# Kernel tuning notes

Measured on AMD Instinct MI355X. Metric: run time of the kernel, lower is better.

Reference implementation:

```python
import jax, jax.numpy as jnp
import numpy as np

B, IN, H = 4096, 1024, 4096
EPS = 1e-5

def setup_inputs() -> dict:
    key = jax.random.key(0)
    ks = jax.random.split(key, 20)
    std = 0.01
    inp = {
        "input": jax.random.normal(ks[0], (B, IN), jnp.float32),
        "max_v": jnp.ones((1,), jnp.float32),
        "min_v": jnp.zeros((1,), jnp.float32),
        "hidden": jax.random.normal(ks[1], (B, 1, H), jnp.float32),
        "Wr_w": std * jax.random.normal(ks[2], (H, IN), jnp.float32),
        "Wr_b": std * jax.random.normal(ks[3], (H,), jnp.float32),
        "Ur_w": std * jax.random.normal(ks[4], (H, H), jnp.float32),
        "Ur_b": std * jax.random.normal(ks[5], (H,), jnp.float32),
        "Wz_w": std * jax.random.normal(ks[6], (H, IN), jnp.float32),
        "Wz_b": std * jax.random.normal(ks[7], (H,), jnp.float32),
        "Uz_w": std * jax.random.normal(ks[8], (H, H), jnp.float32),
        "Uz_b": std * jax.random.normal(ks[9], (H,), jnp.float32),
        "Wh_w": std * jax.random.normal(ks[10], (H, IN), jnp.float32),
        "Wh_b": std * jax.random.normal(ks[11], (H,), jnp.float32),
        "Uh_w": std * jax.random.normal(ks[12], (H, H), jnp.float32),
        "Uh_b": std * jax.random.normal(ks[13], (H,), jnp.float32),
        "out_w": std * jax.random.normal(ks[14], (4, H), jnp.float32),
        "out_b": std * jax.random.normal(ks[15], (4,), jnp.float32),
        "bn_gamma": jnp.ones((1,), jnp.float32),
        "bn_beta": jnp.zeros((1,), jnp.float32),
    }
    return inp

def _lin(x, W, b):
    # x: [B,1,F], W: [O,F] -> [B,1,O]
    return jnp.einsum('blf,of->blo', x, W) + b

def reference(input, max_v, min_v, hidden, Wr_w, Wr_b, Ur_w, Ur_b, Wz_w, Wz_b,
              Uz_w, Uz_b, Wh_w, Wh_b, Uh_w, Uh_b, out_w, out_b, bn_gamma, bn_beta):
    x = input[:, None, :]  # [B,1,IN]
    reset_gate = jax.nn.sigmoid(_lin(x, Wr_w, Wr_b) + _lin(hidden, Ur_w, Ur_b))
    update_gate = jax.nn.sigmoid(_lin(x, Wz_w, Wz_b) + _lin(hidden, Uz_w, Uz_b))
    h_pre = _lin(x, Wh_w, Wh_b) + reset_gate * _lin(hidden, Uh_w, Uh_b)  # [B,1,H]
    # BatchNorm1d(1) in training mode: single channel -> normalize over ALL elements
    mean = jnp.mean(h_pre)
    var = jnp.mean(jnp.square(h_pre - mean))  # biased variance (torch norm uses biased)
    h_bn = (h_pre - mean) * jax.lax.rsqrt(var + EPS) * bn_gamma[0] + bn_beta[0]
    proposal = jax.nn.relu(h_bn)
    current_state = (1.0 - update_gate) * hidden + update_gate * proposal  # [B,1,H]
    out = jnp.einsum('blh,oh->blo', current_state, out_w) + out_b  # [B,1,4]
    return (current_state, out[:, :, 0], out[:, :, 1], out[:, :, 2], out[:, :, 3])
```

## Files before the change

kernel.cpp:

```cpp
#include <hip/hip_runtime.h>

#define HH 4096
#define BB 4096
#define IND 1024
#define NTOT 16777216
#define EPSV 1e-5f

typedef unsigned short u16;
typedef __bf16 bf16x8 __attribute__((ext_vector_type(8)));
typedef float f32x4 __attribute__((ext_vector_type(4)));
typedef u16 u16x8 __attribute__((ext_vector_type(8)));

__device__ __forceinline__ u16 f2bf(float f) {
    unsigned u = __builtin_bit_cast(unsigned, f);
    u += 0x7fffu + ((u >> 16) & 1u);
    return (u16)(u >> 16);
}
__device__ __forceinline__ float bf2f(u16 h) {
    return __builtin_bit_cast(float, ((unsigned)h) << 16);
}

__global__ void cvt_kernel(const float* __restrict__ src, u16* __restrict__ dst, int n) {
    int i4 = (blockIdx.x * blockDim.x + threadIdx.x) * 4;
    int stride = gridDim.x * blockDim.x * 4;
    for (; i4 < n; i4 += stride) {
        f32x4 v = *(const f32x4*)(src + i4);
        u16 o0 = f2bf(v[0]), o1 = f2bf(v[1]), o2 = f2bf(v[2]), o3 = f2bf(v[3]);
        unsigned p0 = (unsigned)o0 | ((unsigned)o1 << 16);
        unsigned p1 = (unsigned)o2 | ((unsigned)o3 << 16);
        *(uint2*)(dst + i4) = make_uint2(p0, p1);
    }
}


__device__ __forceinline__ void stage_tile(const u16* __restrict__ g, int ld, int row0, int k0,
                                           u16* lds, int tid) {
    int l = tid & 63, w = tid >> 6;
#pragma unroll
    for (int jr = 0; jr < 4; ++jr) {
        int offw = jr * 4096 + w * 1024;
        int offl = offw + l * 16;
        int row = offl >> 7;
        int kb = offl & 127;
        const u16* ga = g + (size_t)(row0 + row) * ld + (k0 + (kb >> 1));
        __builtin_amdgcn_global_load_lds(
            (const __attribute__((address_space(1))) unsigned*)ga,
            (__attribute__((address_space(3))) unsigned*)(lds + (offw >> 1)),
            16, 0, 0);
    }
}

__device__ __forceinline__ void zero_acc(f32x4 (&acc)[4][4]) {
#pragma unroll
    for (int i = 0; i < 4; ++i)
#pragma unroll
        for (int j = 0; j < 4; ++j) {
            f32x4 zz = {0.f, 0.f, 0.f, 0.f};
            acc[i][j] = zz;
        }
}

__device__ __forceinline__ void run_phase(const u16* __restrict__ A, int row0a,
                                          const u16* __restrict__ B, int ld, int Klen,
                                          u16* Alds, u16* Blds,
                                          f32x4 (&acc)[4][4], int tid) {
    const int l = tid & 63;
    const int wid = tid >> 6;
    const int wr = wid >> 1, wc = wid & 1;
    const int arow = wr * 64 + (l & 15);
    const int brow = wc * 64 + (l & 15);
    const int kcol = (l >> 4) * 8;
    for (int k0 = 0; k0 < Klen; k0 += 64) {
        stage_tile(A, ld, row0a, k0, Alds, tid);
        stage_tile(B, ld, 0, k0, Blds, tid);
        __syncthreads();
#pragma unroll
        for (int kk = 0; kk < 2; ++kk) {
            bf16x8 af[4], bfr[4];
#pragma unroll
            for (int i = 0; i < 4; ++i)
                af[i] = *(const bf16x8*)(Alds + (arow + i * 16) * 64 + kk * 32 + kcol);
#pragma unroll
            for (int j = 0; j < 4; ++j)
                bfr[j] = *(const bf16x8*)(Blds + (brow + j * 16) * 64 + kk * 32 + kcol);
#pragma unroll
            for (int i = 0; i < 4; ++i)
#pragma unroll
                for (int j = 0; j < 4; ++j)
                    acc[i][j] = __builtin_amdgcn_mfma_f32_16x16x32_bf16(af[i], bfr[j], acc[i][j], 0, 0, 0);
        }
        __syncthreads();
    }
}

__global__ __launch_bounds__(256, 2) void gru_gemm(
    const u16* __restrict__ xbf, const u16* __restrict__ hbf,
    const u16* __restrict__ Wr, const u16* __restrict__ Ur,
    const u16* __restrict__ Wz, const u16* __restrict__ Uz,
    const u16* __restrict__ Wh, const u16* __restrict__ Uh,
    const float* __restrict__ Wr_b, const float* __restrict__ Ur_b,
    const float* __restrict__ Wz_b, const float* __restrict__ Uz_b,
    const float* __restrict__ Wh_b, const float* __restrict__ Uh_b,
    u16* __restrict__ z_out, u16* __restrict__ hpre_out, float* __restrict__ partials) {
    __shared__ __align__(16) u16 Alds[128 * 64];
    __shared__ __align__(16) u16 Blds[128 * 64];
    __shared__ float redS[4], redSS[4];

    const int tid = threadIdx.x;
    const int m0 = blockIdx.x * 128, n0 = blockIdx.y * 128;
    const int l = tid & 63, wid = tid >> 6;
    const int wr = wid >> 1, wc = wid & 1;

    f32x4 acc[4][4];

    zero_acc(acc);
    run_phase(xbf, m0, Wr + (size_t)n0 * IND, IND, IND, Alds, Blds, acc, tid);
    run_phase(hbf, m0, Ur + (size_t)n0 * HH, HH, HH, Alds, Blds, acc, tid);

    float r_st[4][4][4];
#pragma unroll
    for (int j = 0; j < 4; ++j) {
        int col = n0 + wc * 64 + j * 16 + (l & 15);
        float bias = __ldg(Wr_b + col) + __ldg(Ur_b + col);
#pragma unroll
        for (int i = 0; i < 4; ++i)
#pragma unroll
            for (int q = 0; q < 4; ++q)
                r_st[i][j][q] = 1.f / (1.f + __expf(-(acc[i][j][q] + bias)));
    }

    zero_acc(acc);
    run_phase(xbf, m0, Wz + (size_t)n0 * IND, IND, IND, Alds, Blds, acc, tid);
    run_phase(hbf, m0, Uz + (size_t)n0 * HH, HH, HH, Alds, Blds, acc, tid);
#pragma unroll
    for (int j = 0; j < 4; ++j) {
        int col = n0 + wc * 64 + j * 16 + (l & 15);
        float bias = __ldg(Wz_b + col) + __ldg(Uz_b + col);
#pragma unroll
        for (int i = 0; i < 4; ++i) {
            int rowb = m0 + wr * 64 + i * 16 + (l >> 4) * 4;
#pragma unroll
            for (int q = 0; q < 4; ++q) {
                float zv = 1.f / (1.f + __expf(-(acc[i][j][q] + bias)));
                z_out[(size_t)(rowb + q) * HH + col] = f2bf(zv);
            }
        }
    }

    zero_acc(acc);
    run_phase(hbf, m0, Uh + (size_t)n0 * HH, HH, HH, Alds, Blds, acc, tid);
#pragma unroll
    for (int j = 0; j < 4; ++j) {
        int col = n0 + wc * 64 + j * 16 + (l & 15);
        float bias = __ldg(Uh_b + col);
#pragma unroll
        for (int i = 0; i < 4; ++i)
#pragma unroll
            for (int q = 0; q < 4; ++q)
                acc[i][j][q] = r_st[i][j][q] * (acc[i][j][q] + bias);
    }
    run_phase(xbf, m0, Wh + (size_t)n0 * IND, IND, IND, Alds, Blds, acc, tid);

    float s = 0.f, ss = 0.f;
#pragma unroll
    for (int j = 0; j < 4; ++j) {
        int col = n0 + wc * 64 + j * 16 + (l & 15);
        float bias = __ldg(Wh_b + col);
#pragma unroll
        for (int i = 0; i < 4; ++i) {
            int rowb = m0 + wr * 64 + i * 16 + (l >> 4) * 4;
#pragma unroll
            for (int q = 0; q < 4; ++q) {
                float hv = acc[i][j][q] + bias;
                hpre_out[(size_t)(rowb + q) * HH + col] = f2bf(hv);
                s += hv;
                ss += hv * hv;
            }
        }
    }
#pragma unroll
    for (int off = 32; off; off >>= 1) {
        s += __shfl_down(s, off, 64);
        ss += __shfl_down(ss, off, 64);
    }
    if (l == 0) { redS[wid] = s; redSS[wid] = ss; }
    __syncthreads();
    if (tid == 0) {
        int bid = blockIdx.y * gridDim.x + blockIdx.x;
        partials[2 * bid] = redS[0] + redS[1] + redS[2] + redS[3];
        partials[2 * bid + 1] = redSS[0] + redSS[1] + redSS[2] + redSS[3];
    }
}

__global__ void reduce_stats(const float* __restrict__ partials, int nblk,
                             const float* __restrict__ gamma, const float* __restrict__ beta,
                             float* __restrict__ stats) {
    __shared__ float rs[4], rss[4];
    int tid = threadIdx.x;
    float s = 0.f, ss = 0.f;
    for (int i = tid; i < nblk; i += blockDim.x) {
        s += partials[2 * i];
        ss += partials[2 * i + 1];
    }
#pragma unroll
    for (int off = 32; off; off >>= 1) {
        s += __shfl_down(s, off, 64);
        ss += __shfl_down(ss, off, 64);
    }
    if ((tid & 63) == 0) { rs[tid >> 6] = s; rss[tid >> 6] = ss; }
    __syncthreads();
    if (tid == 0) {
        float S = rs[0] + rs[1] + rs[2] + rs[3];
        float SS = rss[0] + rss[1] + rss[2] + rss[3];
        float mean = S / (float)NTOT;
        float var = SS / (float)NTOT - mean * mean;
        float scale = gamma[0] * rsqrtf(var + EPSV);
        stats[0] = scale;
        stats[1] = beta[0] - mean * scale;
    }
}

__global__ __launch_bounds__(256) void finalize(
    const u16* __restrict__ z, const u16* __restrict__ hpre,
    const float* __restrict__ hidden, const float* __restrict__ out_w,
    const float* __restrict__ out_b, const float* __restrict__ stats,
    float* __restrict__ d_out) {
    __shared__ float red[4][4];
    const int b = blockIdx.x, t = threadIdx.x;
    const float scale = stats[0], shift = stats[1];
    const size_t row = (size_t)b * HH;
    float so[4] = {0.f, 0.f, 0.f, 0.f};
#pragma unroll
    for (int jj = 0; jj < 2; ++jj) {
        int h0 = jj * 2048 + t * 8;
        u16x8 zv = *(const u16x8*)(z + row + h0);
        u16x8 hp = *(const u16x8*)(hpre + row + h0);
        f32x4 hd0 = *(const f32x4*)(hidden + row + h0);
        f32x4 hd1 = *(const f32x4*)(hidden + row + h0 + 4);
        f32x4 o0, o1;
#pragma unroll
        for (int e = 0; e < 8; ++e) {
            float zf = bf2f(zv[e]);
            float pv = bf2f(hp[e]) * scale + shift;
            pv = pv > 0.f ? pv : 0.f;
            float hf = (e < 4) ? hd0[e] : hd1[e - 4];
            float cs = (1.f - zf) * hf + zf * pv;
            if (e < 4) o0[e] = cs; else o1[e - 4] = cs;
#pragma unroll
            for (int o = 0; o < 4; ++o)
                so[o] += cs * __ldg(out_w + o * HH + h0 + e);
        }
        *(f32x4*)(d_out + row + h0) = o0;
        *(f32x4*)(d_out + row + h0 + 4) = o1;
    }
#pragma unroll
    for (int off = 32; off; off >>= 1)
#pragma unroll
        for (int o = 0; o < 4; ++o) so[o] += __shfl_down(so[o], off, 64);
    if ((t & 63) == 0)
#pragma unroll
        for (int o = 0; o < 4; ++o) red[t >> 6][o] = so[o];
    __syncthreads();
    if (t < 4) {
        float v = red[0][t] + red[1][t] + red[2][t] + red[3][t] + __ldg(out_b + t);
        d_out[(size_t)NTOT + (size_t)t * BB + b] = v;
    }
}

extern "C" void kernel_launch(void* const* d_in, const int* in_sizes, int n_in,
                              void* d_out, int out_size, void* d_ws, size_t ws_size,
                              hipStream_t stream) {
    const float* input = (const float*)d_in[0];
    const float* hidden = (const float*)d_in[3];
    const float* Wr_w = (const float*)d_in[4];  const float* Wr_b = (const float*)d_in[5];
    const float* Ur_w = (const float*)d_in[6];  const float* Ur_b = (const float*)d_in[7];
    const float* Wz_w = (const float*)d_in[8];  const float* Wz_b = (const float*)d_in[9];
    const float* Uz_w = (const float*)d_in[10]; const float* Uz_b = (const float*)d_in[11];
    const float* Wh_w = (const float*)d_in[12]; const float* Wh_b = (const float*)d_in[13];
    const float* Uh_w = (const float*)d_in[14]; const float* Uh_b = (const float*)d_in[15];
    const float* out_w = (const float*)d_in[16]; const float* out_b = (const float*)d_in[17];
    const float* gamma = (const float*)d_in[18]; const float* beta = (const float*)d_in[19];

    char* ws = (char*)d_ws;
    size_t off = 0;
    auto alloc = [&](size_t bytes) {
        void* p = ws + off;
        off = (off + bytes + 255) & ~(size_t)255;
        return p;
    };
    u16* xbf = (u16*)alloc((size_t)BB * IND * 2);
    u16* hbf = (u16*)alloc((size_t)BB * HH * 2);
    u16* wr = (u16*)alloc((size_t)HH * IND * 2);
    u16* wz = (u16*)alloc((size_t)HH * IND * 2);
    u16* wh = (u16*)alloc((size_t)HH * IND * 2);
    u16* ur = (u16*)alloc((size_t)HH * HH * 2);
    u16* uz = (u16*)alloc((size_t)HH * HH * 2);
    u16* uh = (u16*)alloc((size_t)HH * HH * 2);
    u16* zpl = (u16*)alloc((size_t)BB * HH * 2);
    u16* hpl = (u16*)alloc((size_t)BB * HH * 2);
    float* partials = (float*)alloc(2048 * sizeof(float));
    float* stats = (float*)alloc(16);

    cvt_kernel<<<512, 256, 0, stream>>>(input, xbf, BB * IND);
    cvt_kernel<<<2048, 256, 0, stream>>>(hidden, hbf, BB * HH);
    cvt_kernel<<<512, 256, 0, stream>>>(Wr_w, wr, HH * IND);
    cvt_kernel<<<512, 256, 0, stream>>>(Wz_w, wz, HH * IND);
    cvt_kernel<<<512, 256, 0, stream>>>(Wh_w, wh, HH * IND);
    cvt_kernel<<<2048, 256, 0, stream>>>(Ur_w, ur, HH * HH);
    cvt_kernel<<<2048, 256, 0, stream>>>(Uz_w, uz, HH * HH);
    cvt_kernel<<<2048, 256, 0, stream>>>(Uh_w, uh, HH * HH);

    gru_gemm<<<dim3(32, 32), 256, 0, stream>>>(xbf, hbf, wr, ur, wz, uz, wh, uh,
                                               Wr_b, Ur_b, Wz_b, Uz_b, Wh_b, Uh_b,
                                               zpl, hpl, partials);
    reduce_stats<<<1, 256, 0, stream>>>(partials, 1024, gamma, beta, stats);
    finalize<<<BB, 256, 0, stream>>>(zpl, hpl, hidden, out_w, out_b, stats, (float*)d_out);
}
```

Before: 867.1 us.

## Split fused GRU GEMM into three 256x256-tile pipelined GEMM kernels

Replaces the single fused 128x128-tile kernel, which computed all three gates in sequence, with three launches of a templated 256x256-tile, 512-thread GEMM. The new GEMM uses 128KB of dynamic LDS with double buffering, a swizzled layout, and interleaved global-to-LDS staging with priority-boosted MFMA phases. The reset gate is written as a bf16 plane into the output buffer and read back in the h_pre epilogue. Larger tiles raise arithmetic intensity and the prefetch pipeline hides load latency. The cost is extra global traffic for the r plane and lower occupancy per CU.

```diff
diff --git a/kernel.cpp b/kernel.cpp
--- a/kernel.cpp
+++ b/kernel.cpp
@@ -33,162 +33,229 @@
 }
 
 
-__device__ __forceinline__ void stage_tile(const u16* __restrict__ g, int ld, int row0, int k0,
-                                           u16* lds, int tid) {
-    int l = tid & 63, w = tid >> 6;
-#pragma unroll
-    for (int jr = 0; jr < 4; ++jr) {
-        int offw = jr * 4096 + w * 1024;
-        int offl = offw + l * 16;
-        int row = offl >> 7;
-        int kb = offl & 127;
-        const u16* ga = g + (size_t)(row0 + row) * ld + (k0 + (kb >> 1));
-        __builtin_amdgcn_global_load_lds(
-            (const __attribute__((address_space(1))) unsigned*)ga,
-            (__attribute__((address_space(3))) unsigned*)(lds + (offw >> 1)),
-            16, 0, 0);
-    }
-}
-
-__device__ __forceinline__ void zero_acc(f32x4 (&acc)[4][4]) {
-#pragma unroll
-    for (int i = 0; i < 4; ++i)
+__device__ __forceinline__ int lds_off(int r, int c) {
+    int sub = ((r >> 4) << 1) | (c >> 5);
+    int lin = ((r & 15) << 6) | ((c & 31) << 1);
+    lin ^= (r & 8) << 2;
+    return ((sub << 10) | lin) >> 1;
+}
+
+template<int NT1, int NT2, int EPI>
+__global__ __launch_bounds__(512, 2) void gemm256(
+    const u16* __restrict__ A0, const u16* __restrict__ B0,
+    const u16* __restrict__ A1, const u16* __restrict__ B1,
+    const float* __restrict__ bias_a, const float* __restrict__ bias_b,
+    const u16* __restrict__ rplane, u16* __restrict__ outp,
+    float* __restrict__ partials) {
+    constexpr int NT = NT1 + NT2;
+    constexpr int LD0 = (EPI == 2) ? HH : IND;
+    constexpr int LD1 = (EPI == 2) ? IND : HH;
+    extern __shared__ __align__(16) u16 smem[];
+
+    const int tid = threadIdx.x;
+    const int l = tid & 63, w = tid >> 6;
+    const int lr = l & 15, lq = l >> 4;
+    const int wr = w >> 2;
+    const int wn = w & 3;
+    const int bh = wn >> 1;
+    const int m0 = blockIdx.x * 256, n0 = blockIdx.y * 256;
+    const int linh = ((((lr << 6) | (lq << 4)) ^ ((lr & 8) << 2)) >> 1);
+    const int bsub0 = (wn & 1) * 4;
+
+    auto stageTile = [&](int tt, int mat, int h) {
+        const u16* g = (tt < NT1) ? (mat ? B0 : A0) : (mat ? B1 : A1);
+        const int ld = (tt < NT1) ? LD0 : LD1;
+        const int kb = ((tt < NT1) ? tt : tt - NT1) * 64;
+        const int rowbase = (mat ? n0 : m0) + h * 128;
+        u16* base = smem + (tt & 1) * 32768 + mat * 16384 + h * 8192;
+        const int wq = l << 4;
+        const int lin = wq ^ (((wq >> 9) & 1) << 5);
+        const int rl = lin >> 6;
+        const int cl = (lin & 63) >> 1;
+#pragma unroll
+        for (int j = 0; j < 2; ++j) {
+            const int sub = j * 8 + w;
+            const int r = ((sub >> 1) << 4) | rl;
+            const int c0 = ((sub & 1) << 5) | cl;
+            const u16* ga = g + (size_t)(rowbase + r) * ld + (kb + c0);
+            __builtin_amdgcn_global_load_lds(
+                (const __attribute__((address_space(1))) unsigned*)ga,
+                (__attribute__((address_space(3))) unsigned*)(base + (sub << 9)),
+                16, 0, 0);
+        }
+    };
+
+    f32x4 acc[8][4];
+#pragma unroll
+    for (int i = 0; i < 8; ++i)
 #pragma unroll
         for (int j = 0; j < 4; ++j) {
             f32x4 zz = {0.f, 0.f, 0.f, 0.f};
             acc[i][j] = zz;
         }
-}
-
-__device__ __forceinline__ void run_phase(const u16* __restrict__ A, int row0a,
-                                          const u16* __restrict__ B, int ld, int Klen,
-                                          u16* Alds, u16* Blds,
-                                          f32x4 (&acc)[4][4], int tid) {
-    const int l = tid & 63;
-    const int wid = tid >> 6;
-    const int wr = wid >> 1, wc = wid & 1;
-    const int arow = wr * 64 + (l & 15);
-    const int brow = wc * 64 + (l & 15);
-    const int kcol = (l >> 4) * 8;
-    for (int k0 = 0; k0 < Klen; k0 += 64) {
-        stage_tile(A, ld, row0a, k0, Alds, tid);
-        stage_tile(B, ld, 0, k0, Blds, tid);
+
+    stageTile(0, 0, 0); stageTile(0, 0, 1); stageTile(0, 1, 0); stageTile(0, 1, 1);
+    stageTile(1, 0, 0); stageTile(1, 0, 1);
+    asm volatile("s_waitcnt vmcnt(4)" ::: "memory");
+    __builtin_amdgcn_s_barrier();
+
+    bf16x8 a0[4][2], a1[4][2], bb[2][2];
+
+    for (int t = 0; t < NT; ++t) {
+        const u16* Ah = smem + (t & 1) * 32768 + wr * 8192 + linh;
+        const u16* Bh = smem + (t & 1) * 32768 + 16384 + bh * 8192 + linh;
+        int t1 = t + 1; if (t1 == NT) t1 = 0;
+        int t2 = t + 2; if (t2 >= NT) t2 -= NT;
+
+#pragma unroll
+        for (int i = 0; i < 4; ++i)
+#pragma unroll
+            for (int ks = 0; ks < 2; ++ks)
+                a0[i][ks] = *(const bf16x8*)(Ah + (i * 2 + ks) * 512);
+#pragma unroll
+        for (int n = 0; n < 2; ++n)
+#pragma unroll
+            for (int ks = 0; ks < 2; ++ks)
+                bb[n][ks] = *(const bf16x8*)(Bh + ((bsub0 + n) * 2 + ks) * 512);
+        stageTile(t1, 1, 0);
+        __builtin_amdgcn_s_barrier();
+        asm volatile("s_waitcnt lgkmcnt(0)" ::: "memory");
+        __builtin_amdgcn_sched_barrier(0);
+        __builtin_amdgcn_s_setprio(1);
+#pragma unroll
+        for (int ks = 0; ks < 2; ++ks)
+#pragma unroll
+            for (int i = 0; i < 4; ++i)
+#pragma unroll
+                for (int n = 0; n < 2; ++n)
+                    acc[i][n] = __builtin_amdgcn_mfma_f32_16x16x32_bf16(a0[i][ks], bb[n][ks], acc[i][n], 0, 0, 0);
+        __builtin_amdgcn_s_setprio(0);
+        __builtin_amdgcn_s_barrier();
+
+#pragma unroll
+        for (int i = 0; i < 4; ++i)
+#pragma unroll
+            for (int ks = 0; ks < 2; ++ks)
+                a1[i][ks] = *(const bf16x8*)(Ah + 4096 + (i * 2 + ks) * 512);
+        stageTile(t1, 1, 1);
+        __builtin_amdgcn_s_barrier();
+        asm volatile("s_waitcnt lgkmcnt(0)" ::: "memory");
+        __builtin_amdgcn_sched_barrier(0);
+        __builtin_amdgcn_s_setprio(1);
+#pragma unroll
+        for (int ks = 0; ks < 2; ++ks)
+#pragma unroll
+            for (int i = 0; i < 4; ++i)
+#pragma unroll
+                for (int n = 0; n < 2; ++n)
+                    acc[4 + i][n] = __builtin_amdgcn_mfma_f32_16x16x32_bf16(a1[i][ks], bb[n][ks], acc[4 + i][n], 0, 0, 0);
+        __builtin_amdgcn_s_setprio(0);
+        __builtin_amdgcn_s_barrier();
+
+#pragma unroll
+        for (int n = 0; n < 2; ++n)
+#pragma unroll
+            for (int ks = 0; ks < 2; ++ks)
+                bb[n][ks] = *(const bf16x8*)(Bh + ((bsub0 + 2 + n) * 2 + ks) * 512);
+        stageTile(t2, 0, 0);
+        __builtin_amdgcn_s_barrier();
+        asm volatile("s_waitcnt lgkmcnt(0)" ::: "memory");
+        __builtin_amdgcn_sched_barrier(0);
+        __builtin_amdgcn_s_setprio(1);
+#pragma unroll
+        for (int ks = 0; ks < 2; ++ks)
+#pragma unroll
+            for (int i = 0; i < 4; ++i)
+#pragma unroll
+                for (int n = 0; n < 2; ++n)
+                    acc[i][2 + n] = __builtin_amdgcn_mfma_f32_16x16x32_bf16(a0[i][ks], bb[n][ks], acc[i][2 + n], 0, 0, 0);
+        __builtin_amdgcn_s_setprio(0);
+        __builtin_amdgcn_s_barrier();
+
+        stageTile(t2, 0, 1);
+        asm volatile("s_waitcnt vmcnt(4)" ::: "memory");
+        __builtin_amdgcn_s_barrier();
+        __builtin_amdgcn_s_setprio(1);
+#pragma unroll
+        for (int ks = 0; ks < 2; ++ks)
+#pragma unroll
+            for (int i = 0; i < 4; ++i)
+#pragma unroll
+                for (int n = 0; n < 2; ++n)
+                    acc[4 + i][2 + n] = __builtin_amdgcn_mfma_f32_16x16x32_bf16(a1[i][ks], bb[n][ks], acc[4 + i][2 + n], 0, 0, 0);
+        __builtin_amdgcn_s_setprio(0);
+        if constexpr (EPI == 2) {
+            if (t == NT1 - 1) {
+#pragma unroll
+                for (int m8 = 0; m8 < 8; ++m8) {
+                    const int rowb = m0 + wr * 128 + m8 * 16 + lq * 4;
+#pragma unroll
+                    for (int n8 = 0; n8 < 4; ++n8) {
+                        const int col = n0 + wn * 64 + n8 * 16 + lr;
+                        const float bias = bias_a[col];
+#pragma unroll
+                        for (int q = 0; q < 4; ++q) {
+                            float rv = bf2f(rplane[(size_t)(rowb + q) * HH + col]);
+                            acc[m8][n8][q] = rv * (acc[m8][n8][q] + bias);
+                        }
+                    }
+                }
+            }
+        }
+        __builtin_amdgcn_s_barrier();
+    }
+
+    if constexpr (EPI == 2) {
+        float s = 0.f, ss = 0.f;
+#pragma unroll
+        for (int m8 = 0; m8 < 8; ++m8) {
+            const int rowb = m0 + wr * 128 + m8 * 16 + lq * 4;
+#pragma unroll
+            for (int n8 = 0; n8 < 4; ++n8) {
+                const int col = n0 + wn * 64 + n8 * 16 + lr;
+                const float bias = bias_b[col];
+#pragma unroll
+                for (int q = 0; q < 4; ++q) {
+                    float v = acc[m8][n8][q] + bias;
+                    outp[(size_t)(rowb + q) * HH + col] = f2bf(v);
+                    s += v; ss += v * v;
+                }
+            }
+        }
+#pragma unroll
+        for (int off = 32; off; off >>= 1) {
+            s += __shfl_down(s, off, 64);
+            ss += __shfl_down(ss, off, 64);
+        }
+        asm volatile("s_waitcnt vmcnt(0)" ::: "memory");
         __syncthreads();
-#pragma unroll
-        for (int kk = 0; kk < 2; ++kk) {
-            bf16x8 af[4], bfr[4];
-#pragma unroll
-            for (int i = 0; i < 4; ++i)
-                af[i] = *(const bf16x8*)(Alds + (arow + i * 16) * 64 + kk * 32 + kcol);
-#pragma unroll
-            for (int j = 0; j < 4; ++j)
-                bfr[j] = *(const bf16x8*)(Blds + (brow + j * 16) * 64 + kk * 32 + kcol);
-#pragma unroll
-            for (int i = 0; i < 4; ++i)
-#pragma unroll
-                for (int j = 0; j < 4; ++j)
-                    acc[i][j] = __builtin_amdgcn_mfma_f32_16x16x32_bf16(af[i], bfr[j], acc[i][j], 0, 0, 0);
-        }
+        float* red = (float*)smem;
+        if (l == 0) { red[w * 2] = s; red[w * 2 + 1] = ss; }
         __syncthreads();
-    }
-}
-
-__global__ __launch_bounds__(256, 2) void gru_gemm(
-    const u16* __restrict__ xbf, const u16* __restrict__ hbf,
-    const u16* __restrict__ Wr, const u16* __restrict__ Ur,
-    const u16* __restrict__ Wz, const u16* __restrict__ Uz,
-    const u16* __restrict__ Wh, const u16* __restrict__ Uh,
-    const float* __restrict__ Wr_b, const float* __restrict__ Ur_b,
-    const float* __restrict__ Wz_b, const float* __restrict__ Uz_b,
-    const float* __restrict__ Wh_b, const float* __restrict__ Uh_b,
-    u16* __restrict__ z_out, u16* __restrict__ hpre_out, float* __restrict__ partials) {
-    __shared__ __align__(16) u16 Alds[128 * 64];
-    __shared__ __align__(16) u16 Blds[128 * 64];
-    __shared__ float redS[4], redSS[4];
-
-    const int tid = threadIdx.x;
-    const int m0 = blockIdx.x * 128, n0 = blockIdx.y * 128;
-    const int l = tid & 63, wid = tid >> 6;
-    const int wr = wid >> 1, wc = wid & 1;
-
-    f32x4 acc[4][4];
-
-    zero_acc(acc);
-    run_phase(xbf, m0, Wr + (size_t)n0 * IND, IND, IND, Alds, Blds, acc, tid);
-    run_phase(hbf, m0, Ur + (size_t)n0 * HH, HH, HH, Alds, Blds, acc, tid);
-
-    float r_st[4][4][4];
-#pragma unroll
-    for (int j = 0; j < 4; ++j) {
-        int col = n0 + wc * 64 + j * 16 + (l & 15);
-        float bias = __ldg(Wr_b + col) + __ldg(Ur_b + col);
-#pragma unroll
-        for (int i = 0; i < 4; ++i)
-#pragma unroll
-            for (int q = 0; q < 4; ++q)
-                r_st[i][j][q] = 1.f / (1.f + __expf(-(acc[i][j][q] + bias)));
-    }
-
-    zero_acc(acc);
-    run_phase(xbf, m0, Wz + (size_t)n0 * IND, IND, IND, Alds, Blds, acc, tid);
-    run_phase(hbf, m0, Uz + (size_t)n0 * HH, HH, HH, Alds, Blds, acc, tid);
-#pragma unroll
-    for (int j = 0; j < 4; ++j) {
-        int col = n0 + wc * 64 + j * 16 + (l & 15);
-        float bias = __ldg(Wz_b + col) + __ldg(Uz_b + col);
-#pragma unroll
-        for (int i = 0; i < 4; ++i) {
-            int rowb = m0 + wr * 64 + i * 16 + (l >> 4) * 4;
-#pragma unroll
-            for (int q = 0; q < 4; ++q) {
-                float zv = 1.f / (1.f + __expf(-(acc[i][j][q] + bias)));
-                z_out[(size_t)(rowb + q) * HH + col] = f2bf(zv);
+        if (tid == 0) {
+            float S = 0.f, SS = 0.f;
+#pragma unroll
+            for (int i = 0; i < 8; ++i) { S += red[2 * i]; SS += red[2 * i + 1]; }
+            const int bid = blockIdx.y * 16 + blockIdx.x;
+            partials[2 * bid] = S;
+            partials[2 * bid + 1] = SS;
+        }
+    } else {
+#pragma unroll
+        for (int m8 = 0; m8 < 8; ++m8) {
+            const int rowb = m0 + wr * 128 + m8 * 16 + lq * 4;
+#pragma unroll
+            for (int n8 = 0; n8 < 4; ++n8) {
+                const int col = n0 + wn * 64 + n8 * 16 + lr;
+                const float bias = bias_a[col] + bias_b[col];
+#pragma unroll
+                for (int q = 0; q < 4; ++q) {
+                    float v = 1.f / (1.f + __expf(-(acc[m8][n8][q] + bias)));
+                    outp[(size_t)(rowb + q) * HH + col] = f2bf(v);
+                }
             }
         }
-    }
-
-    zero_acc(acc);
-    run_phase(hbf, m0, Uh + (size_t)n0 * HH, HH, HH, Alds, Blds, acc, tid);
-#pragma unroll
-    for (int j = 0; j < 4; ++j) {
-        int col = n0 + wc * 64 + j * 16 + (l & 15);
-        float bias = __ldg(Uh_b + col);
-#pragma unroll
-        for (int i = 0; i < 4; ++i)
-#pragma unroll
-            for (int q = 0; q < 4; ++q)
-                acc[i][j][q] = r_st[i][j][q] * (acc[i][j][q] + bias);
-    }
-    run_phase(xbf, m0, Wh + (size_t)n0 * IND, IND, IND, Alds, Blds, acc, tid);
-
-    float s = 0.f, ss = 0.f;
-#pragma unroll
-    for (int j = 0; j < 4; ++j) {
-        int col = n0 + wc * 64 + j * 16 + (l & 15);
-        float bias = __ldg(Wh_b + col);
-#pragma unroll
-        for (int i = 0; i < 4; ++i) {
-            int rowb = m0 + wr * 64 + i * 16 + (l >> 4) * 4;
-#pragma unroll
-            for (int q = 0; q < 4; ++q) {
-                float hv = acc[i][j][q] + bias;
-                hpre_out[(size_t)(rowb + q) * HH + col] = f2bf(hv);
-                s += hv;
-                ss += hv * hv;
-            }
-        }
-    }
-#pragma unroll
-    for (int off = 32; off; off >>= 1) {
-        s += __shfl_down(s, off, 64);
-        ss += __shfl_down(ss, off, 64);
-    }
-    if (l == 0) { redS[wid] = s; redSS[wid] = ss; }
-    __syncthreads();
-    if (tid == 0) {
-        int bid = blockIdx.y * gridDim.x + blockIdx.x;
-        partials[2 * bid] = redS[0] + redS[1] + redS[2] + redS[3];
-        partials[2 * bid + 1] = redSS[0] + redSS[1] + redSS[2] + redSS[3];
+        asm volatile("s_waitcnt vmcnt(0)" ::: "memory");
     }
 }
 
@@ -290,29 +357,39 @@
     };
     u16* xbf = (u16*)alloc((size_t)BB * IND * 2);
     u16* hbf = (u16*)alloc((size_t)BB * HH * 2);
-    u16* wr = (u16*)alloc((size_t)HH * IND * 2);
-    u16* wz = (u16*)alloc((size_t)HH * IND * 2);
-    u16* wh = (u16*)alloc((size_t)HH * IND * 2);
-    u16* ur = (u16*)alloc((size_t)HH * HH * 2);
-    u16* uz = (u16*)alloc((size_t)HH * HH * 2);
-    u16* uh = (u16*)alloc((size_t)HH * HH * 2);
+    u16* wrp = (u16*)alloc((size_t)HH * IND * 2);
+    u16* wzp = (u16*)alloc((size_t)HH * IND * 2);
+    u16* whp = (u16*)alloc((size_t)HH * IND * 2);
+    u16* urp = (u16*)alloc((size_t)HH * HH * 2);
+    u16* uzp = (u16*)alloc((size_t)HH * HH * 2);
+    u16* uhp = (u16*)alloc((size_t)HH * HH * 2);
     u16* zpl = (u16*)alloc((size_t)BB * HH * 2);
     u16* hpl = (u16*)alloc((size_t)BB * HH * 2);
     float* partials = (float*)alloc(2048 * sizeof(float));
     float* stats = (float*)alloc(16);
 
+    u16* rpl = (u16*)d_out;
+
+    hipFuncSetAttribute((const void*)gemm256<16, 64, 0>, hipFuncAttributeMaxDynamicSharedMemorySize, 131072);
+    hipFuncSetAttribute((const void*)gemm256<16, 64, 1>, hipFuncAttributeMaxDynamicSharedMemorySize, 131072);
+    hipFuncSetAttribute((const void*)gemm256<64, 16, 2>, hipFuncAttributeMaxDynamicSharedMemorySize, 131072);
+
     cvt_kernel<<<512, 256, 0, stream>>>(input, xbf, BB * IND);
     cvt_kernel<<<2048, 256, 0, stream>>>(hidden, hbf, BB * HH);
-    cvt_kernel<<<512, 256, 0, stream>>>(Wr_w, wr, HH * IND);
-    cvt_kernel<<<512, 256, 0, stream>>>(Wz_w, wz, HH * IND);
-    cvt_kernel<<<512, 256, 0, stream>>>(Wh_w, wh, HH * IND);
-    cvt_kernel<<<2048, 256, 0, stream>>>(Ur_w, ur, HH * HH);
-    cvt_kernel<<<2048, 256, 0, stream>>>(Uz_w, uz, HH * HH);
-    cvt_kernel<<<2048, 256, 0, stream>>>(Uh_w, uh, HH * HH);
-
-    gru_gemm<<<dim3(32, 32), 256, 0, stream>>>(xbf, hbf, wr, ur, wz, uz, wh, uh,
-                                               Wr_b, Ur_b, Wz_b, Uz_b, Wh_b, Uh_b,
-                                               zpl, hpl, partials);
-    reduce_stats<<<1, 256, 0, stream>>>(partials, 1024, gamma, beta, stats);
+    cvt_kernel<<<512, 256, 0, stream>>>(Wr_w, wrp, HH * IND);
+    cvt_kernel<<<512, 256, 0, stream>>>(Wz_w, wzp, HH * IND);
+    cvt_kernel<<<512, 256, 0, stream>>>(Wh_w, whp, HH * IND);
+    cvt_kernel<<<2048, 256, 0, stream>>>(Ur_w, urp, HH * HH);
+    cvt_kernel<<<2048, 256, 0, stream>>>(Uz_w, uzp, HH * HH);
+    cvt_kernel<<<2048, 256, 0, stream>>>(Uh_w, uhp, HH * HH);
+
+    gemm256<16, 64, 0><<<dim3(16, 16), 512, 131072, stream>>>(
+        xbf, wrp, hbf, urp, Wr_b, Ur_b, nullptr, rpl, partials);
+    gemm256<16, 64, 1><<<dim3(16, 16), 512, 131072, stream>>>(
+        xbf, wzp, hbf, uzp, Wz_b, Uz_b, nullptr, zpl, partials);
+    gemm256<64, 16, 2><<<dim3(16, 16), 512, 131072, stream>>>(
+        hbf, uhp, xbf, whp, Uh_b, Wh_b, rpl, hpl, partials);
+
+    reduce_stats<<<1, 256, 0, stream>>>(partials, 256, gamma, beta, stats);
     finalize<<<BB, 256, 0, stream>>>(zpl, hpl, hidden, out_w, out_b, stats, (float*)d_out);
 }
```

New measurement: 827.9 us. 4.5% less time.

## Swizzle LDS tile layout and remap workgroups across XCDs in GRU GEMM

Applied to the files above, without the earlier changes.

Stores each staged tile in LDS as 16x32 sub-blocks with an XOR swizzle and rewrites the fragment reads to match. The goal is to remove bank conflicts on the bf16x8 reads that feed the MFMA instructions. The launch becomes a 1D grid, and each block index is remapped so that consecutive blocks dispatched to the same XCD share output tiles, which should improve L2 reuse of the A and B operands. The address math is subtle, so a swizzle mismatch would silently give wrong results.

```diff
diff --git a/kernel.cpp b/kernel.cpp
--- a/kernel.cpp
+++ b/kernel.cpp
@@ -35,17 +35,18 @@
 
 __device__ __forceinline__ void stage_tile(const u16* __restrict__ g, int ld, int row0, int k0,
                                            u16* lds, int tid) {
-    int l = tid & 63, w = tid >> 6;
-#pragma unroll
-    for (int jr = 0; jr < 4; ++jr) {
-        int offw = jr * 4096 + w * 1024;
-        int offl = offw + l * 16;
-        int row = offl >> 7;
-        int kb = offl & 127;
-        const u16* ga = g + (size_t)(row0 + row) * ld + (k0 + (kb >> 1));
+    const int l = tid & 63, w = tid >> 6;
+#pragma unroll
+    for (int j = 0; j < 4; ++j) {
+        const int sub = j * 4 + w;
+        const int d = l << 4;
+        const int lin = d ^ (((d >> 9) & 1) << 5);
+        const int r = ((sub >> 1) << 4) | (lin >> 6);
+        const int c = ((sub & 1) << 5) | ((lin & 63) >> 1);
+        const u16* ga = g + (size_t)(row0 + r) * ld + (k0 + c);
         __builtin_amdgcn_global_load_lds(
             (const __attribute__((address_space(1))) unsigned*)ga,
-            (__attribute__((address_space(3))) unsigned*)(lds + (offw >> 1)),
+            (__attribute__((address_space(3))) unsigned*)(lds + (sub << 9)),
             16, 0, 0);
     }
 }
@@ -67,9 +68,8 @@
     const int l = tid & 63;
     const int wid = tid >> 6;
     const int wr = wid >> 1, wc = wid & 1;
-    const int arow = wr * 64 + (l & 15);
-    const int brow = wc * 64 + (l & 15);
-    const int kcol = (l >> 4) * 8;
+    const int lr = l & 15, lq = l >> 4;
+    const int swzh = (((lr << 6) | (lq << 4)) ^ ((lr & 8) << 2)) >> 1;
     for (int k0 = 0; k0 < Klen; k0 += 64) {
         stage_tile(A, ld, row0a, k0, Alds, tid);
         stage_tile(B, ld, 0, k0, Blds, tid);
@@ -79,10 +79,10 @@
             bf16x8 af[4], bfr[4];
 #pragma unroll
             for (int i = 0; i < 4; ++i)
-                af[i] = *(const bf16x8*)(Alds + (arow + i * 16) * 64 + kk * 32 + kcol);
+                af[i] = *(const bf16x8*)(Alds + ((wr * 8 + i * 2 + kk) << 9) + swzh);
 #pragma unroll
             for (int j = 0; j < 4; ++j)
-                bfr[j] = *(const bf16x8*)(Blds + (brow + j * 16) * 64 + kk * 32 + kcol);
+                bfr[j] = *(const bf16x8*)(Blds + ((wc * 8 + j * 2 + kk) << 9) + swzh);
 #pragma unroll
             for (int i = 0; i < 4; ++i)
 #pragma unroll
@@ -107,7 +107,9 @@
     __shared__ float redS[4], redSS[4];
 
     const int tid = threadIdx.x;
-    const int m0 = blockIdx.x * 128, n0 = blockIdx.y * 128;
+    const int bid = blockIdx.x;
+    const int wg = (bid & 7) * 128 + (bid >> 3);
+    const int m0 = (wg & 31) * 128, n0 = (wg >> 5) * 128;
     const int l = tid & 63, wid = tid >> 6;
     const int wr = wid >> 1, wc = wid & 1;
 
@@ -186,7 +188,6 @@
     if (l == 0) { redS[wid] = s; redSS[wid] = ss; }
     __syncthreads();
     if (tid == 0) {
-        int bid = blockIdx.y * gridDim.x + blockIdx.x;
         partials[2 * bid] = redS[0] + redS[1] + redS[2] + redS[3];
         partials[2 * bid + 1] = redSS[0] + redSS[1] + redSS[2] + redSS[3];
     }
@@ -310,9 +311,9 @@
     cvt_kernel<<<2048, 256, 0, stream>>>(Uz_w, uz, HH * HH);
     cvt_kernel<<<2048, 256, 0, stream>>>(Uh_w, uh, HH * HH);
 
-    gru_gemm<<<dim3(32, 32), 256, 0, stream>>>(xbf, hbf, wr, ur, wz, uz, wh, uh,
-                                               Wr_b, Ur_b, Wz_b, Uz_b, Wh_b, Uh_b,
-                                               zpl, hpl, partials);
+    gru_gemm<<<1024, 256, 0, stream>>>(xbf, hbf, wr, ur, wz, uz, wh, uh,
+                                       Wr_b, Ur_b, Wz_b, Uz_b, Wh_b, Uh_b,
+                                       zpl, hpl, partials);
     reduce_stats<<<1, 256, 0, stream>>>(partials, 1024, gamma, beta, stats);
     finalize<<<BB, 256, 0, stream>>>(zpl, hpl, hidden, out_w, out_b, stats, (float*)d_out);
 }
```

Measured after the change: 884.9 us. +2.1%, slower.
